# Optimization experiments

Measured on AMD Instinct MI355X. Metric: run time of the kernel, lower is better.

Reference implementation:

```python
import jax, jax.numpy as jnp
import numpy as np

N_QUBITS = 4
DIM = 2 ** N_QUBITS  # 16 statevector amplitudes


def _cnot_perm(c, t):
    # CNOT(control=c, target=t) is a permutation of basis states (its own inverse).
    # wire 0 is the most-significant bit (default.qubit convention).
    perm = np.arange(DIM)
    for k in range(DIM):
        if (k >> (N_QUBITS - 1 - c)) & 1:
            perm[k] = k ^ (1 << (N_QUBITS - 1 - t))
    return perm

CNOT_PERMS = [jnp.asarray(_cnot_perm(q, (q + 1) % N_QUBITS)) for q in range(N_QUBITS)]
# Z_SIGNS[q, k] = +1 if qubit q is |0> in basis state k else -1
Z_SIGNS = jnp.asarray(
    np.array([[1.0 - 2.0 * ((k >> (N_QUBITS - 1 - q)) & 1) for k in range(DIM)]
              for q in range(N_QUBITS)], dtype=np.float32))


def _apply_rx(state, theta, q):
    # state: (N, 16) complex64; theta: scalar or (N,); q: wire index
    n = state.shape[0]
    st = state.reshape(n, 2 ** q, 2, 2 ** (N_QUBITS - 1 - q))
    a0, a1 = st[:, :, 0, :], st[:, :, 1, :]
    c = jnp.reshape(jnp.cos(theta * 0.5), (-1, 1, 1))
    s = jnp.reshape(jnp.sin(theta * 0.5), (-1, 1, 1))
    new0 = c * a0 - 1j * s * a1
    new1 = c * a1 - 1j * s * a0
    return jnp.stack([new0, new1], axis=2).reshape(n, DIM)


def _quantum(angles, params):
    # angles: (N, 4) float32 input rotations; params: (4,) learned rotations
    n = angles.shape[0]
    state = jnp.zeros((n, DIM), jnp.complex64).at[:, 0].set(1.0)
    for q in range(N_QUBITS):
        state = _apply_rx(state, angles[:, q], q)
    for q in range(N_QUBITS):
        state = _apply_rx(state, params[q], q)
        state = state[:, CNOT_PERMS[q]]  # CNOT(q, (q+1)%4)
    probs = state.real ** 2 + state.imag ** 2  # (N, 16)
    return probs @ Z_SIGNS.T  # (N, 4) expvals of PauliZ


def setup_inputs() -> dict:
    key = jax.random.key(0)
    kx, kwi, kbi, kwo, kbo, kp = jax.random.split(key, 6)
    B, S, D = 16, 2048, 1024
    lim_i = 1.0 / np.sqrt(D)
    lim_o = 1.0 / np.sqrt(N_QUBITS)
    return {
        "x": jax.random.normal(kx, (B, S, D), jnp.float32),
        "Wi": jax.random.uniform(kwi, (D, N_QUBITS), jnp.float32, -lim_i, lim_i),
        "bi": jax.random.uniform(kbi, (N_QUBITS,), jnp.float32, -lim_i, lim_i),
        "Wo": jax.random.uniform(kwo, (N_QUBITS, D), jnp.float32, -lim_o, lim_o),
        "bo": jax.random.uniform(kbo, (D,), jnp.float32, -lim_o, lim_o),
        "ffn_params": jax.random.normal(kp, (N_QUBITS,), jnp.float32) * 0.1,
    }


def reference(x, Wi, bi, Wo, bo, ffn_params):
    B, S, D = x.shape
    xp = x @ Wi + bi                                  # (B, S, 4)
    mn = xp.min(axis=-1, keepdims=True)
    mx = xp.max(axis=-1, keepdims=True)
    ang = (xp - mn) / (mx - mn + 1e-8) * jnp.pi       # per-token min-max scale to [0, pi]
    q = _quantum(ang.reshape(-1, N_QUBITS), ffn_params).reshape(B, S, N_QUBITS)
    return q @ Wo + bo                                # (B, S, D); dropout = identity (eval)
```

## Files before the change

### kernel.cpp

```cpp
#include <hip/hip_runtime.h>

#define NQ      4
#define DIMQ    16
#define D_MODEL 1024
#define TPB     64
#define CHUNK   128
#define NCHUNK  8
#define LROW    132
#define PI_F    3.14159265358979323846f

__global__ __launch_bounds__(256, 2)
void qffn_kernel(const float* __restrict__ x,
                 const float* __restrict__ Wi,
                 const float* __restrict__ bi,
                 const float* __restrict__ Wo,
                 const float* __restrict__ bo,
                 const float* __restrict__ fp,
                 float* __restrict__ out,
                 int n_tokens)
{
    __shared__ float s_x[TPB * LROW];
    __shared__ float s_wi[D_MODEL * 4];
    __shared__ float s_pq[4 * TPB * 4];
    __shared__ float s_q[TPB * 4];

    const int tid  = threadIdx.x;
    const int lane = tid & 63;
    const int w    = tid >> 6;
    const int tile = blockIdx.x * TPB;

    float pc[NQ], ps[NQ];
    #pragma unroll
    for (int q = 0; q < NQ; ++q) {
        float h = 0.5f * fp[q];
        pc[q] = __cosf(h);
        ps[q] = __sinf(h);
    }
    const float bi0 = bi[0], bi1 = bi[1], bi2 = bi[2], bi3 = bi[3];

    const float4* Wo4 = (const float4*)Wo;
    const float4 wo0 = Wo4[0 * 256 + tid];
    const float4 wo1 = Wo4[1 * 256 + tid];
    const float4 wo2 = Wo4[2 * 256 + tid];
    const float4 wo3 = Wo4[3 * 256 + tid];
    const float4 bo4 = ((const float4*)bo)[tid];

    {
        const float4* Wi4 = (const float4*)Wi;
        float4* s_wi4 = (float4*)s_wi;
        #pragma unroll
        for (int k = 0; k < 4; ++k) s_wi4[tid + k * 256] = Wi4[tid + k * 256];
    }

    const float4* x4 = (const float4*)x;
    float4 xr[8];
    #pragma unroll
    for (int i = 0; i < 8; ++i) {
        int flat = tid + i * 256;
        int row = flat >> 5, col4 = flat & 31;
        int grow = tile + row; if (grow > n_tokens - 1) grow = n_tokens - 1;
        xr[i] = x4[grow * 256 + col4];
    }

    float p0 = 0.f, p1 = 0.f, p2 = 0.f, p3 = 0.f;

    for (int c = 0; c < NCHUNK; ++c) {
        #pragma unroll
        for (int i = 0; i < 8; ++i) {
            int flat = tid + i * 256;
            int row = flat >> 5, col4 = flat & 31;
            *(float4*)&s_x[row * LROW + col4 * 4] = xr[i];
        }
        __syncthreads();
        if (c + 1 < NCHUNK) {
            #pragma unroll
            for (int i = 0; i < 8; ++i) {
                int flat = tid + i * 256;
                int row = flat >> 5, col4 = flat & 31;
                int grow = tile + row; if (grow > n_tokens - 1) grow = n_tokens - 1;
                xr[i] = x4[grow * 256 + (c + 1) * 32 + col4];
            }
        }
        const float*  xrow = &s_x[lane * LROW + w * 32];
        const float4* wv4  = (const float4*)&s_wi[(c * CHUNK + w * 32) * 4];
        #pragma unroll
        for (int j4 = 0; j4 < 8; ++j4) {
            float4 xv = *(const float4*)(xrow + j4 * 4);
            float4 wa = wv4[j4 * 4 + 0];
            float4 wb = wv4[j4 * 4 + 1];
            float4 wc = wv4[j4 * 4 + 2];
            float4 wd = wv4[j4 * 4 + 3];
            p0 = fmaf(xv.x, wa.x, p0); p1 = fmaf(xv.x, wa.y, p1); p2 = fmaf(xv.x, wa.z, p2); p3 = fmaf(xv.x, wa.w, p3);
            p0 = fmaf(xv.y, wb.x, p0); p1 = fmaf(xv.y, wb.y, p1); p2 = fmaf(xv.y, wb.z, p2); p3 = fmaf(xv.y, wb.w, p3);
            p0 = fmaf(xv.z, wc.x, p0); p1 = fmaf(xv.z, wc.y, p1); p2 = fmaf(xv.z, wc.z, p2); p3 = fmaf(xv.z, wc.w, p3);
            p0 = fmaf(xv.w, wd.x, p0); p1 = fmaf(xv.w, wd.y, p1); p2 = fmaf(xv.w, wd.z, p2); p3 = fmaf(xv.w, wd.w, p3);
        }
        __syncthreads();
    }

    *(float4*)&s_pq[tid * 4] = make_float4(p0, p1, p2, p3);
    __syncthreads();

    float4 a0 = *(const float4*)&s_pq[(0 * 64 + lane) * 4];
    float4 a1 = *(const float4*)&s_pq[(1 * 64 + lane) * 4];
    float4 a2 = *(const float4*)&s_pq[(2 * 64 + lane) * 4];
    float4 a3 = *(const float4*)&s_pq[(3 * 64 + lane) * 4];
    float xp0 = a0.x + a1.x + a2.x + a3.x + bi0;
    float xp1 = a0.y + a1.y + a2.y + a3.y + bi1;
    float xp2 = a0.z + a1.z + a2.z + a3.z + bi2;
    float xp3 = a0.w + a1.w + a2.w + a3.w + bi3;

    float mn = fminf(fminf(xp0, xp1), fminf(xp2, xp3));
    float mx = fmaxf(fmaxf(xp0, xp1), fmaxf(xp2, xp3));
    float inv = PI_F / (mx - mn + 1e-8f);
    float ang[NQ];
    ang[0] = (xp0 - mn) * inv;
    ang[1] = (xp1 - mn) * inv;
    ang[2] = (xp2 - mn) * inv;
    ang[3] = (xp3 - mn) * inv;

    float sr[DIMQ], si[DIMQ];
    #pragma unroll
    for (int k = 0; k < DIMQ; ++k) { sr[k] = (k == 0) ? 1.0f : 0.0f; si[k] = 0.0f; }

    #pragma unroll
    for (int q = 0; q < NQ; ++q) {
        const int bit = 8 >> q;
        float h = 0.5f * ang[q];
        float cth = __cosf(h), sth = __sinf(h);
        #pragma unroll
        for (int k = 0; k < DIMQ; ++k) {
            if (!(k & bit)) {
                const int k1 = k | bit;
                float a0r = sr[k],  a0i = si[k];
                float a1r = sr[k1], a1i = si[k1];
                sr[k]  = fmaf(cth, a0r,  sth * a1i);
                si[k]  = fmaf(cth, a0i, -sth * a1r);
                sr[k1] = fmaf(cth, a1r,  sth * a0i);
                si[k1] = fmaf(cth, a1i, -sth * a0r);
            }
        }
    }
    #pragma unroll
    for (int q = 0; q < NQ; ++q) {
        const int bit = 8 >> q;
        float cth = pc[q], sth = ps[q];
        #pragma unroll
        for (int k = 0; k < DIMQ; ++k) {
            if (!(k & bit)) {
                const int k1 = k | bit;
                float a0r = sr[k],  a0i = si[k];
                float a1r = sr[k1], a1i = si[k1];
                sr[k]  = fmaf(cth, a0r,  sth * a1i);
                si[k]  = fmaf(cth, a0i, -sth * a1r);
                sr[k1] = fmaf(cth, a1r,  sth * a0i);
                si[k1] = fmaf(cth, a1i, -sth * a0r);
            }
        }
        const int cbit = 8 >> q;
        const int tbit = 8 >> ((q + 1) & 3);
        #pragma unroll
        for (int k = 0; k < DIMQ; ++k) {
            if ((k & cbit) && !(k & tbit)) {
                const int k1 = k | tbit;
                float t;
                t = sr[k]; sr[k] = sr[k1]; sr[k1] = t;
                t = si[k]; si[k] = si[k1]; si[k1] = t;
            }
        }
    }

    float pr[DIMQ];
    #pragma unroll
    for (int k = 0; k < DIMQ; ++k) pr[k] = fmaf(sr[k], sr[k], si[k] * si[k]);

    float qv0 = 0.f, qv1 = 0.f, qv2 = 0.f, qv3 = 0.f;
    #pragma unroll
    for (int k = 0; k < DIMQ; ++k) {
        qv0 += (k & 8) ? -pr[k] : pr[k];
        qv1 += (k & 4) ? -pr[k] : pr[k];
        qv2 += (k & 2) ? -pr[k] : pr[k];
        qv3 += (k & 1) ? -pr[k] : pr[k];
    }

    if (tid < 64) *(float4*)&s_q[lane * 4] = make_float4(qv0, qv1, qv2, qv3);
    __syncthreads();

    float4* out4 = (float4*)out;
    #pragma unroll 4
    for (int i = 0; i < TPB; ++i) {
        int grow = tile + i;
        if (grow < n_tokens) {
            float4 qq = *(const float4*)&s_q[i * 4];
            float4 v;
            v.x = fmaf(qq.x, wo0.x, fmaf(qq.y, wo1.x, fmaf(qq.z, wo2.x, fmaf(qq.w, wo3.x, bo4.x))));
            v.y = fmaf(qq.x, wo0.y, fmaf(qq.y, wo1.y, fmaf(qq.z, wo2.y, fmaf(qq.w, wo3.y, bo4.y))));
            v.z = fmaf(qq.x, wo0.z, fmaf(qq.y, wo1.z, fmaf(qq.z, wo2.z, fmaf(qq.w, wo3.z, bo4.z))));
            v.w = fmaf(qq.x, wo0.w, fmaf(qq.y, wo1.w, fmaf(qq.z, wo2.w, fmaf(qq.w, wo3.w, bo4.w))));
            out4[grow * 256 + tid] = v;
        }
    }
}

extern "C" void kernel_launch(void* const* d_in, const int* in_sizes, int n_in,
                              void* d_out, int out_size, void* d_ws, size_t ws_size,
                              hipStream_t stream)
{
    (void)d_ws; (void)ws_size; (void)n_in; (void)out_size;
    const float* x  = (const float*)d_in[0];
    const float* Wi = (const float*)d_in[1];
    const float* bi = (const float*)d_in[2];
    const float* Wo = (const float*)d_in[3];
    const float* bo = (const float*)d_in[4];
    const float* fp = (const float*)d_in[5];
    float* out = (float*)d_out;

    int n_tokens = in_sizes[0] / D_MODEL;
    int grid = (n_tokens + TPB - 1) / TPB;
    qffn_kernel<<<grid, 256, 0, stream>>>(x, Wi, bi, Wo, bo, fp, out, n_tokens);
}
```

Measured before the change: 258.0 us.

## Compute input projection per-wave with register-held Wi and shuffle reductions

Replaces the shared-memory staged x tiles and Wi copy with a scheme where each wave handles 16 tokens. Each lane loads its slice of the row directly from global memory, multiplies it against Wi held in registers, and reduces across the wave with xor shuffles. This removes the large LDS footprint and the per-chunk barriers, and launch bounds are raised to allow 4 blocks per CU. Costs: 64 registers for Wi, 24 shuffle steps per token, and the quantum simulation restricted to the first wave.

```diff
diff --git a/kernel.cpp b/kernel.cpp
--- a/kernel.cpp
+++ b/kernel.cpp
@@ -4,12 +4,9 @@
 #define DIMQ    16
 #define D_MODEL 1024
 #define TPB     64
-#define CHUNK   128
-#define NCHUNK  8
-#define LROW    132
 #define PI_F    3.14159265358979323846f
 
-__global__ __launch_bounds__(256, 2)
+__global__ __launch_bounds__(256, 4)
 void qffn_kernel(const float* __restrict__ x,
                  const float* __restrict__ Wi,
                  const float* __restrict__ bi,
@@ -19,9 +16,7 @@
                  float* __restrict__ out,
                  int n_tokens)
 {
-    __shared__ float s_x[TPB * LROW];
-    __shared__ float s_wi[D_MODEL * 4];
-    __shared__ float s_pq[4 * TPB * 4];
+    __shared__ float s_xp[TPB * 4];
     __shared__ float s_q[TPB * 4];
 
     const int tid  = threadIdx.x;
@@ -29,14 +24,54 @@
     const int w    = tid >> 6;
     const int tile = blockIdx.x * TPB;
 
-    float pc[NQ], ps[NQ];
+    const float4* x4  = (const float4*)x;
+    const float4* Wi4 = (const float4*)Wi;
+
+    float4 wi[4][4];
     #pragma unroll
-    for (int q = 0; q < NQ; ++q) {
-        float h = 0.5f * fp[q];
-        pc[q] = __cosf(h);
-        ps[q] = __sinf(h);
+    for (int c = 0; c < 4; ++c) {
+        #pragma unroll
+        for (int e = 0; e < 4; ++e)
+            wi[c][e] = Wi4[(c * 64 + lane) * 4 + e];
     }
     const float bi0 = bi[0], bi1 = bi[1], bi2 = bi[2], bi3 = bi[3];
+
+    float k0 = 0.f, k1 = 0.f, k2 = 0.f, k3 = 0.f;
+
+    #define DOT4(xe, wv) \
+        p0 = fmaf(xe, wv.x, p0); p1 = fmaf(xe, wv.y, p1); \
+        p2 = fmaf(xe, wv.z, p2); p3 = fmaf(xe, wv.w, p3);
+
+    #pragma unroll 2
+    for (int t = 0; t < 16; ++t) {
+        int tok = tile + w * 16 + t;
+        if (tok > n_tokens - 1) tok = n_tokens - 1;
+        const size_t base = (size_t)tok * 256;
+        float4 xv0 = x4[base + 0 * 64 + lane];
+        float4 xv1 = x4[base + 1 * 64 + lane];
+        float4 xv2 = x4[base + 2 * 64 + lane];
+        float4 xv3 = x4[base + 3 * 64 + lane];
+
+        float p0 = 0.f, p1 = 0.f, p2 = 0.f, p3 = 0.f;
+        DOT4(xv0.x, wi[0][0]) DOT4(xv0.y, wi[0][1]) DOT4(xv0.z, wi[0][2]) DOT4(xv0.w, wi[0][3])
+        DOT4(xv1.x, wi[1][0]) DOT4(xv1.y, wi[1][1]) DOT4(xv1.z, wi[1][2]) DOT4(xv1.w, wi[1][3])
+        DOT4(xv2.x, wi[2][0]) DOT4(xv2.y, wi[2][1]) DOT4(xv2.z, wi[2][2]) DOT4(xv2.w, wi[2][3])
+        DOT4(xv3.x, wi[3][0]) DOT4(xv3.y, wi[3][1]) DOT4(xv3.z, wi[3][2]) DOT4(xv3.w, wi[3][3])
+
+        #pragma unroll
+        for (int m = 1; m < 64; m <<= 1) {
+            p0 += __shfl_xor(p0, m, 64);
+            p1 += __shfl_xor(p1, m, 64);
+            p2 += __shfl_xor(p2, m, 64);
+            p3 += __shfl_xor(p3, m, 64);
+        }
+        if (lane == t) { k0 = p0; k1 = p1; k2 = p2; k3 = p3; }
+    }
+
+    if (lane < 16) {
+        *(float4*)&s_xp[(w * 16 + lane) * 4] =
+            make_float4(k0 + bi0, k1 + bi1, k2 + bi2, k3 + bi3);
+    }
 
     const float4* Wo4 = (const float4*)Wo;
     const float4 wo0 = Wo4[0 * 256 + tid];
@@ -45,149 +80,99 @@
     const float4 wo3 = Wo4[3 * 256 + tid];
     const float4 bo4 = ((const float4*)bo)[tid];
 
-    {
-        const float4* Wi4 = (const float4*)Wi;
-        float4* s_wi4 = (float4*)s_wi;
-        #pragma unroll
-        for (int k = 0; k < 4; ++k) s_wi4[tid + k * 256] = Wi4[tid + k * 256];
-    }
-
-    const float4* x4 = (const float4*)x;
-    float4 xr[8];
-    #pragma unroll
-    for (int i = 0; i < 8; ++i) {
-        int flat = tid + i * 256;
-        int row = flat >> 5, col4 = flat & 31;
-        int grow = tile + row; if (grow > n_tokens - 1) grow = n_tokens - 1;
-        xr[i] = x4[grow * 256 + col4];
-    }
-
-    float p0 = 0.f, p1 = 0.f, p2 = 0.f, p3 = 0.f;
-
-    for (int c = 0; c < NCHUNK; ++c) {
-        #pragma unroll
-        for (int i = 0; i < 8; ++i) {
-            int flat = tid + i * 256;
-            int row = flat >> 5, col4 = flat & 31;
-            *(float4*)&s_x[row * LROW + col4 * 4] = xr[i];
-        }
-        __syncthreads();
-        if (c + 1 < NCHUNK) {
+    __syncthreads();
+
+    if (tid < 64) {
+        float4 xpv = *(const float4*)&s_xp[tid * 4];
+        float xp0 = xpv.x, xp1 = xpv.y, xp2 = xpv.z, xp3 = xpv.w;
+
+        float pc[NQ], ps[NQ];
+        #pragma unroll
+        for (int q = 0; q < NQ; ++q) {
+            float h = 0.5f * fp[q];
+            pc[q] = __cosf(h);
+            ps[q] = __sinf(h);
+        }
+
+        float mn = fminf(fminf(xp0, xp1), fminf(xp2, xp3));
+        float mx = fmaxf(fmaxf(xp0, xp1), fmaxf(xp2, xp3));
+        float inv = PI_F / (mx - mn + 1e-8f);
+        float ang[NQ];
+        ang[0] = (xp0 - mn) * inv;
+        ang[1] = (xp1 - mn) * inv;
+        ang[2] = (xp2 - mn) * inv;
+        ang[3] = (xp3 - mn) * inv;
+
+        float sr[DIMQ], si[DIMQ];
+        #pragma unroll
+        for (int k = 0; k < DIMQ; ++k) { sr[k] = (k == 0) ? 1.0f : 0.0f; si[k] = 0.0f; }
+
+        #pragma unroll
+        for (int q = 0; q < NQ; ++q) {
+            const int bit = 8 >> q;
+            float h = 0.5f * ang[q];
+            float cth = __cosf(h), sth = __sinf(h);
             #pragma unroll
-            for (int i = 0; i < 8; ++i) {
-                int flat = tid + i * 256;
-                int row = flat >> 5, col4 = flat & 31;
-                int grow = tile + row; if (grow > n_tokens - 1) grow = n_tokens - 1;
-                xr[i] = x4[grow * 256 + (c + 1) * 32 + col4];
+            for (int k = 0; k < DIMQ; ++k) {
+                if (!(k & bit)) {
+                    const int k1 = k | bit;
+                    float a0r = sr[k],  a0i = si[k];
+                    float a1r = sr[k1], a1i = si[k1];
+                    sr[k]  = fmaf(cth, a0r,  sth * a1i);
+                    si[k]  = fmaf(cth, a0i, -sth * a1r);
+                    sr[k1] = fmaf(cth, a1r,  sth * a0i);
+                    si[k1] = fmaf(cth, a1i, -sth * a0r);
+                }
             }
         }
-        const float*  xrow = &s_x[lane * LROW + w * 32];
-        const float4* wv4  = (const float4*)&s_wi[(c * CHUNK + w * 32) * 4];
-        #pragma unroll
-        for (int j4 = 0; j4 < 8; ++j4) {
-            float4 xv = *(const float4*)(xrow + j4 * 4);
-            float4 wa = wv4[j4 * 4 + 0];
-            float4 wb = wv4[j4 * 4 + 1];
-            float4 wc = wv4[j4 * 4 + 2];
-            float4 wd = wv4[j4 * 4 + 3];
-            p0 = fmaf(xv.x, wa.x, p0); p1 = fmaf(xv.x, wa.y, p1); p2 = fmaf(xv.x, wa.z, p2); p3 = fmaf(xv.x, wa.w, p3);
-            p0 = fmaf(xv.y, wb.x, p0); p1 = fmaf(xv.y, wb.y, p1); p2 = fmaf(xv.y, wb.z, p2); p3 = fmaf(xv.y, wb.w, p3);
-            p0 = fmaf(xv.z, wc.x, p0); p1 = fmaf(xv.z, wc.y, p1); p2 = fmaf(xv.z, wc.z, p2); p3 = fmaf(xv.z, wc.w, p3);
-            p0 = fmaf(xv.w, wd.x, p0); p1 = fmaf(xv.w, wd.y, p1); p2 = fmaf(xv.w, wd.z, p2); p3 = fmaf(xv.w, wd.w, p3);
-        }
-        __syncthreads();
-    }
-
-    *(float4*)&s_pq[tid * 4] = make_float4(p0, p1, p2, p3);
+        #pragma unroll
+        for (int q = 0; q < NQ; ++q) {
+            const int bit = 8 >> q;
+            float cth = pc[q], sth = ps[q];
+            #pragma unroll
+            for (int k = 0; k < DIMQ; ++k) {
+                if (!(k & bit)) {
+                    const int k1 = k | bit;
+                    float a0r = sr[k],  a0i = si[k];
+                    float a1r = sr[k1], a1i = si[k1];
+                    sr[k]  = fmaf(cth, a0r,  sth * a1i);
+                    si[k]  = fmaf(cth, a0i, -sth * a1r);
+                    sr[k1] = fmaf(cth, a1r,  sth * a0i);
+                    si[k1] = fmaf(cth, a1i, -sth * a0r);
+                }
+            }
+            const int cbit = 8 >> q;
+            const int tbit = 8 >> ((q + 1) & 3);
+            #pragma unroll
+            for (int k = 0; k < DIMQ; ++k) {
+                if ((k & cbit) && !(k & tbit)) {
+                    const int k1 = k | tbit;
+                    float t;
+                    t = sr[k]; sr[k] = sr[k1]; sr[k1] = t;
+                    t = si[k]; si[k] = si[k1]; si[k1] = t;
+                }
+            }
+        }
+
+        float pr[DIMQ];
+        #pragma unroll
+        for (int k = 0; k < DIMQ; ++k) pr[k] = fmaf(sr[k], sr[k], si[k] * si[k]);
+
+        float qv0 = 0.f, qv1 = 0.f, qv2 = 0.f, qv3 = 0.f;
+        #pragma unroll
+        for (int k = 0; k < DIMQ; ++k) {
+            qv0 += (k & 8) ? -pr[k] : pr[k];
+            qv1 += (k & 4) ? -pr[k] : pr[k];
+            qv2 += (k & 2) ? -pr[k] : pr[k];
+            qv3 += (k & 1) ? -pr[k] : pr[k];
+        }
+        *(float4*)&s_q[tid * 4] = make_float4(qv0, qv1, qv2, qv3);
+    }
+
     __syncthreads();
 
-    float4 a0 = *(const float4*)&s_pq[(0 * 64 + lane) * 4];
-    float4 a1 = *(const float4*)&s_pq[(1 * 64 + lane) * 4];
-    float4 a2 = *(const float4*)&s_pq[(2 * 64 + lane) * 4];
-    float4 a3 = *(const float4*)&s_pq[(3 * 64 + lane) * 4];
-    float xp0 = a0.x + a1.x + a2.x + a3.x + bi0;
-    float xp1 = a0.y + a1.y + a2.y + a3.y + bi1;
-    float xp2 = a0.z + a1.z + a2.z + a3.z + bi2;
-    float xp3 = a0.w + a1.w + a2.w + a3.w + bi3;
-
-    float mn = fminf(fminf(xp0, xp1), fminf(xp2, xp3));
-    float mx = fmaxf(fmaxf(xp0, xp1), fmaxf(xp2, xp3));
-    float inv = PI_F / (mx - mn + 1e-8f);
-    float ang[NQ];
-    ang[0] = (xp0 - mn) * inv;
-    ang[1] = (xp1 - mn) * inv;
-    ang[2] = (xp2 - mn) * inv;
-    ang[3] = (xp3 - mn) * inv;
-
-    float sr[DIMQ], si[DIMQ];
-    #pragma unroll
-    for (int k = 0; k < DIMQ; ++k) { sr[k] = (k == 0) ? 1.0f : 0.0f; si[k] = 0.0f; }
-
-    #pragma unroll
-    for (int q = 0; q < NQ; ++q) {
-        const int bit = 8 >> q;
-        float h = 0.5f * ang[q];
-        float cth = __cosf(h), sth = __sinf(h);
-        #pragma unroll
-        for (int k = 0; k < DIMQ; ++k) {
-            if (!(k & bit)) {
-                const int k1 = k | bit;
-                float a0r = sr[k],  a0i = si[k];
-                float a1r = sr[k1], a1i = si[k1];
-                sr[k]  = fmaf(cth, a0r,  sth * a1i);
-                si[k]  = fmaf(cth, a0i, -sth * a1r);
-                sr[k1] = fmaf(cth, a1r,  sth * a0i);
-                si[k1] = fmaf(cth, a1i, -sth * a0r);
-            }
-        }
-    }
-    #pragma unroll
-    for (int q = 0; q < NQ; ++q) {
-        const int bit = 8 >> q;
-        float cth = pc[q], sth = ps[q];
-        #pragma unroll
-        for (int k = 0; k < DIMQ; ++k) {
-            if (!(k & bit)) {
-                const int k1 = k | bit;
-                float a0r = sr[k],  a0i = si[k];
-                float a1r = sr[k1], a1i = si[k1];
-                sr[k]  = fmaf(cth, a0r,  sth * a1i);
-                si[k]  = fmaf(cth, a0i, -sth * a1r);
-                sr[k1] = fmaf(cth, a1r,  sth * a0i);
-                si[k1] = fmaf(cth, a1i, -sth * a0r);
-            }
-        }
-        const int cbit = 8 >> q;
-        const int tbit = 8 >> ((q + 1) & 3);
-        #pragma unroll
-        for (int k = 0; k < DIMQ; ++k) {
-            if ((k & cbit) && !(k & tbit)) {
-                const int k1 = k | tbit;
-                float t;
-                t = sr[k]; sr[k] = sr[k1]; sr[k1] = t;
-                t = si[k]; si[k] = si[k1]; si[k1] = t;
-            }
-        }
-    }
-
-    float pr[DIMQ];
-    #pragma unroll
-    for (int k = 0; k < DIMQ; ++k) pr[k] = fmaf(sr[k], sr[k], si[k] * si[k]);
-
-    float qv0 = 0.f, qv1 = 0.f, qv2 = 0.f, qv3 = 0.f;
-    #pragma unroll
-    for (int k = 0; k < DIMQ; ++k) {
-        qv0 += (k & 8) ? -pr[k] : pr[k];
-        qv1 += (k & 4) ? -pr[k] : pr[k];
-        qv2 += (k & 2) ? -pr[k] : pr[k];
-        qv3 += (k & 1) ? -pr[k] : pr[k];
-    }
-
-    if (tid < 64) *(float4*)&s_q[lane * 4] = make_float4(qv0, qv1, qv2, qv3);
-    __syncthreads();
-
     float4* out4 = (float4*)out;
-    #pragma unroll 4
+    #pragma unroll 8
     for (int i = 0; i < TPB; ++i) {
         int grow = tile + i;
         if (grow < n_tokens) {
@@ -197,7 +182,7 @@
             v.y = fmaf(qq.x, wo0.y, fmaf(qq.y, wo1.y, fmaf(qq.z, wo2.y, fmaf(qq.w, wo3.y, bo4.y))));
             v.z = fmaf(qq.x, wo0.z, fmaf(qq.y, wo1.z, fmaf(qq.z, wo2.z, fmaf(qq.w, wo3.z, bo4.z))));
             v.w = fmaf(qq.x, wo0.w, fmaf(qq.y, wo1.w, fmaf(qq.z, wo2.w, fmaf(qq.w, wo3.w, bo4.w))));
-            out4[grow * 256 + tid] = v;
+            out4[(size_t)grow * 256 + tid] = v;
         }
     }
 }
```

After: 242.5 us. 1.06x faster.
